# Kernel optimization log

Hardware: AMD Instinct MI355X
Metric: run time of the kernel (lower is better)

The kernel has to match this reference:

```python
import jax, jax.numpy as jnp
import numpy as np

N_NODES = 40000
N_EDGES = 640000
F_IN = 128
HID = 128
N_CLASSES = 10
N_GRAPHS = 64


def _gcn_conv(x, row, col, norm, W, b, n_nodes):
    h = x @ W                                   # [N, H]
    msg = h[row] * norm[:, None]                # [E+N, H] gather + scale
    out = jax.ops.segment_sum(msg, col, num_segments=n_nodes)  # scatter-add
    return out + b


def setup_inputs() -> dict:
    key = jax.random.key(0)
    ks = jax.random.split(key, 8)
    x = jax.random.normal(ks[0], (N_NODES, F_IN), dtype=jnp.float32)
    edge_index = jax.random.randint(ks[1], (2, N_EDGES), 0, N_NODES, dtype=jnp.int32)
    batch = jnp.sort(jax.random.randint(ks[2], (N_NODES,), 0, N_GRAPHS, dtype=jnp.int32))
    s1 = 1.0 / np.sqrt(F_IN)
    s2 = 1.0 / np.sqrt(HID)
    W1 = jax.random.normal(ks[3], (F_IN, HID), dtype=jnp.float32) * s1
    W2 = jax.random.normal(ks[4], (HID, HID), dtype=jnp.float32) * s2
    W3 = jax.random.normal(ks[5], (HID, HID), dtype=jnp.float32) * s2
    Wl = jax.random.normal(ks[6], (HID, N_CLASSES), dtype=jnp.float32) * s2
    b1 = jnp.zeros((HID,), jnp.float32)
    b2 = jnp.zeros((HID,), jnp.float32)
    b3 = jnp.zeros((HID,), jnp.float32)
    bl = jnp.zeros((N_CLASSES,), jnp.float32)
    return {"x": x, "edge_index": edge_index, "batch": batch,
            "W1": W1, "b1": b1, "W2": W2, "b2": b2, "W3": W3, "b3": b3,
            "Wl": Wl, "bl": bl}


def reference(x, edge_index, batch, W1, b1, W2, b2, W3, b3, Wl, bl):
    n = x.shape[0]
    # add self-loops (PyG add_remaining_self_loops with weight 1)
    loops = jnp.arange(n, dtype=edge_index.dtype)
    row = jnp.concatenate([edge_index[0], loops])
    col = jnp.concatenate([edge_index[1], loops])
    w = jnp.ones(row.shape, dtype=x.dtype)
    # symmetric normalization: deg over target nodes incl. self-loops
    deg = jax.ops.segment_sum(w, col, num_segments=n)
    dis = jnp.where(deg > 0, jax.lax.rsqrt(deg), 0.0)
    norm = dis[row] * dis[col]                  # [E+N]

    h = jax.nn.relu(_gcn_conv(x, row, col, norm, W1, b1, n))
    h = jax.nn.relu(_gcn_conv(h, row, col, norm, W2, b2, n))
    h = jax.nn.relu(_gcn_conv(h, row, col, norm, W3, b3, n))

    # global mean pool over graph ids
    sums = jax.ops.segment_sum(h, batch, num_segments=N_GRAPHS)      # [G, H]
    cnts = jax.ops.segment_sum(jnp.ones((n,), h.dtype), batch, num_segments=N_GRAPHS)
    pooled = sums / jnp.maximum(cnts, 1.0)[:, None]
    # dropout(p=0.2) is identity in eval mode
    return pooled @ Wl + bl                     # [G, num_classes]
```

## Files before the change

kernel.cpp:

```cpp
#include <hip/hip_runtime.h>
#include <hip/hip_bf16.h>

#define N_NODES   40000
#define N_EDGES   640000
#define F         128
#define N_GRAPHS  64
#define N_CLASSES 10

typedef short bf16x8 __attribute__((ext_vector_type(8)));
typedef float f32x4  __attribute__((ext_vector_type(4)));

__device__ __forceinline__ unsigned short f2bf(float f) {
    union { float f; unsigned u; } v; v.f = f;
    unsigned r = v.u + 0x7fffu + ((v.u >> 16) & 1u);
    return (unsigned short)(r >> 16);
}
__device__ __forceinline__ float bflo(unsigned u) { return __uint_as_float(u << 16); }
__device__ __forceinline__ float bfhi(unsigned u) { return __uint_as_float(u & 0xffff0000u); }
__device__ __forceinline__ unsigned pack2(float a, float b) {
    return (unsigned)f2bf(a) | ((unsigned)f2bf(b) << 16);
}

#define APITCH 136

__global__ void wcvt_kernel(const float* __restrict__ W1, const float* __restrict__ W2,
                            const float* __restrict__ W3, unsigned short* __restrict__ Wt,
                            int* __restrict__ deg, int* __restrict__ tks) {
    int idx = blockIdx.x * 256 + threadIdx.x;
    if (idx < N_NODES) deg[idx] = 0;
    if (idx < 2) tks[idx] = 0;
    int l = idx >> 14;
    int r = idx & 16383;
    int c = r >> 7, k = r & 127;
    const float* W = (l == 0) ? W1 : ((l == 1) ? W2 : W3);
    Wt[idx] = f2bf(W[k * 128 + c]);
}

#define SCAN_BLOCKS 40
#define SCAN_CHUNK  1000
__global__ __launch_bounds__(256) void scan_kernel(
    const int* __restrict__ deg, int* __restrict__ rowptr,
    int* __restrict__ cursor, float* __restrict__ dis,
    float* __restrict__ pooled_zero, int* __restrict__ chunkSum,
    int* __restrict__ ticket) {
    __shared__ int wpart[4];
    __shared__ int blockBase;
    const int tid  = threadIdx.x;
    const int lane = tid & 63;
    const int wave = tid >> 6;
    const int b    = blockIdx.x;
    const int base = b * SCAN_CHUNK;

    for (int k = b * 256 + tid; k < N_GRAPHS * F + N_GRAPHS; k += SCAN_BLOCKS * 256)
        pooled_zero[k] = 0.f;

    int4 d = make_int4(0, 0, 0, 0);
    if (tid < 250) d = *(const int4*)(deg + base + tid * 4);
    const int sown = d.x + d.y + d.z + d.w;

    int s = sown;
#pragma unroll
    for (int off = 1; off < 64; off <<= 1) {
        int n = __shfl_up(s, off, 64);
        if (lane >= off) s += n;
    }
    if (lane == 63) wpart[wave] = s;
    __syncthreads();

    if (tid == 0) {
        int run = 0;
#pragma unroll
        for (int w = 0; w < 4; ++w) { int t = wpart[w]; wpart[w] = run; run += t; }
        atomicExch(&chunkSum[b], run);
        __threadfence();
        atomicAdd(ticket, 1);
        while (atomicAdd(ticket, 0) < SCAN_BLOCKS) { }
    }
    __syncthreads();

    if (wave == 0) {
        int cs = (lane < SCAN_BLOCKS) ? atomicAdd(&chunkSum[lane], 0) : 0;
        int sc_ = cs;
#pragma unroll
        for (int off = 1; off < 64; off <<= 1) {
            int n = __shfl_up(sc_, off, 64);
            if (lane >= off) sc_ += n;
        }
        int bb = __shfl(sc_, (b == 0) ? 0 : b - 1, 64);
        if (lane == 0) blockBase = (b == 0) ? 0 : bb;
    }
    __syncthreads();

    if (tid < 250) {
        int excl = blockBase + wpart[wave] + (s - sown);
        int4 r;
        r.x = excl;
        r.y = r.x + d.x;
        r.z = r.y + d.y;
        r.w = r.z + d.z;
        *(int4*)(rowptr + base + tid * 4) = r;
        *(int4*)(cursor + base + tid * 4) = r;
        float4 di;
        di.x = rsqrtf((float)d.x + 1.0f);
        di.y = rsqrtf((float)d.y + 1.0f);
        di.z = rsqrtf((float)d.z + 1.0f);
        di.w = rsqrtf((float)d.w + 1.0f);
        *(float4*)(dis + base + tid * 4) = di;
    }
}

__global__ void fill_kernel(const int* __restrict__ row, const int* __restrict__ col,
                            int* __restrict__ cursor, int* __restrict__ csr_src) {
    int e = blockIdx.x * 256 + threadIdx.x;
    if (e < N_EDGES) {
        int pos = atomicAdd(&cursor[col[e]], 1);
        csr_src[pos] = row[e];
    }
}

template<bool ABF16, bool RELU, bool SCALE, bool COUNT>
__global__ __launch_bounds__(256) void gemm_mfma(
    const void* __restrict__ Araw, const unsigned short* __restrict__ Wt,
    const float* __restrict__ bias, const float* __restrict__ dis,
    unsigned short* __restrict__ Hb,
    const int* __restrict__ cnt_col, int* __restrict__ cnt_deg) {
    __shared__ unsigned short As[64 * APITCH];
    __shared__ unsigned short Ws[64 * APITCH];
    const int tid  = threadIdx.x;
    const int row0 = blockIdx.x * 64;

    if (COUNT) {
        int t = (blockIdx.x * 256 + tid) * 4;
#pragma unroll
        for (int j = 0; j < 4; ++j) atomicAdd(&cnt_deg[cnt_col[t + j]], 1);
    }

    {
        const uint4* src = (const uint4*)Wt;
#pragma unroll
        for (int j = 0; j < 4; ++j) {
            int c4 = tid + j * 256;
            int c  = c4 >> 4;
            int o  = c4 & 15;
            *(uint4*)(Ws + c * APITCH + o * 8) = src[c4];
        }
    }
    if (ABF16) {
        const uint4* src = (const uint4*)Araw;
#pragma unroll
        for (int j = 0; j < 4; ++j) {
            int c4 = tid + j * 256;
            int r  = c4 >> 4;
            int p  = c4 & 15;
            int o  = p << 3;
            uint4 hv = src[(size_t)(row0 + r) * 16 + p];
            float f0 = bflo(hv.x), f1 = bfhi(hv.x), f2 = bflo(hv.y), f3 = bfhi(hv.y);
            float f4_ = bflo(hv.z), f5 = bfhi(hv.z), f6 = bflo(hv.w), f7 = bfhi(hv.w);
            if (bias) {
                float4 b0 = *(const float4*)(bias + o);
                float4 b1 = *(const float4*)(bias + o + 4);
                f0 += b0.x; f1 += b0.y; f2 += b0.z; f3 += b0.w;
                f4_ += b1.x; f5 += b1.y; f6 += b1.z; f7 += b1.w;
            }
            if (RELU) {
                f0 = fmaxf(f0, 0.f); f1 = fmaxf(f1, 0.f); f2 = fmaxf(f2, 0.f);
                f3 = fmaxf(f3, 0.f); f4_ = fmaxf(f4_, 0.f); f5 = fmaxf(f5, 0.f);
                f6 = fmaxf(f6, 0.f); f7 = fmaxf(f7, 0.f);
            }
            uint4 pk;
            pk.x = pack2(f0, f1); pk.y = pack2(f2, f3);
            pk.z = pack2(f4_, f5); pk.w = pack2(f6, f7);
            *(uint4*)(As + r * APITCH + o) = pk;
        }
    } else {
        const float* A = (const float*)Araw;
#pragma unroll
        for (int j = 0; j < 8; ++j) {
            int c4 = tid + j * 256;
            int r  = c4 >> 5;
            int o  = (c4 & 31) << 2;
            float4 v = *(const float4*)(A + (size_t)(row0 + r) * F + o);
            if (bias) {
                v.x += bias[o + 0]; v.y += bias[o + 1];
                v.z += bias[o + 2]; v.w += bias[o + 3];
            }
            if (RELU) {
                v.x = fmaxf(v.x, 0.f); v.y = fmaxf(v.y, 0.f);
                v.z = fmaxf(v.z, 0.f); v.w = fmaxf(v.w, 0.f);
            }
            uint2 p;
            p.x = pack2(v.x, v.y);
            p.y = pack2(v.z, v.w);
            *(uint2*)(As + r * APITCH + o) = p;
        }
    }
    __syncthreads();

    const int lane = tid & 63;
    const int wave = tid >> 6;
    const int m16  = lane & 15;
    const int quad = lane >> 4;

    f32x4 acc[8];
#pragma unroll
    for (int t = 0; t < 8; ++t) acc[t] = (f32x4)(0.0f);

    bf16x8 afrag[4];
#pragma unroll
    for (int kk = 0; kk < 4; ++kk)
        afrag[kk] = *(const bf16x8*)(As + (wave * 16 + m16) * APITCH + kk * 32 + quad * 8);

#pragma unroll
    for (int kk = 0; kk < 4; ++kk) {
#pragma unroll
        for (int t = 0; t < 4; ++t) {
            bf16x8 b = *(const bf16x8*)(Ws + (t * 16 + m16) * APITCH + kk * 32 + quad * 8);
            acc[t] = __builtin_amdgcn_mfma_f32_16x16x32_bf16(afrag[kk], b, acc[t], 0, 0, 0);
        }
    }
    __syncthreads();

    {
        const uint4* src = (const uint4*)Wt + 1024;
#pragma unroll
        for (int j = 0; j < 4; ++j) {
            int c4 = tid + j * 256;
            int c  = c4 >> 4;
            int o  = c4 & 15;
            *(uint4*)(Ws + c * APITCH + o * 8) = src[c4];
        }
    }
    __syncthreads();

#pragma unroll
    for (int kk = 0; kk < 4; ++kk) {
#pragma unroll
        for (int t = 0; t < 4; ++t) {
            bf16x8 b = *(const bf16x8*)(Ws + (t * 16 + m16) * APITCH + kk * 32 + quad * 8);
            acc[4 + t] = __builtin_amdgcn_mfma_f32_16x16x32_bf16(afrag[kk], b, acc[4 + t], 0, 0, 0);
        }
    }

    const int rloc = wave * 16 + quad * 4;
    float sc[4];
#pragma unroll
    for (int rg = 0; rg < 4; ++rg) sc[rg] = SCALE ? dis[row0 + rloc + rg] : 1.0f;
#pragma unroll
    for (int t = 0; t < 8; ++t) {
        int col = t * 16 + m16;
#pragma unroll
        for (int rg = 0; rg < 4; ++rg)
            As[(rloc + rg) * APITCH + col] = f2bf(acc[t][rg] * sc[rg]);
    }
#pragma unroll
    for (int i = 0; i < 4; ++i) {
        int idx = lane + i * 64;
        int r   = idx >> 4;
        int p   = idx & 15;
        uint4 val = *(const uint4*)(As + (wave * 16 + r) * APITCH + p * 8);
        *((uint4*)(Hb + (size_t)(row0 + wave * 16 + r) * F) + p) = val;
    }
}

template <bool SCALED>
__global__ __launch_bounds__(256) void gather_kernel(
    const unsigned short* __restrict__ Hb, const int* __restrict__ csr_src,
    const int* __restrict__ rowptr, const int* __restrict__ deg,
    const float* __restrict__ dis, unsigned short* __restrict__ AGGb) {
    const int gid  = blockIdx.x * 256 + threadIdx.x;
    const int v    = gid >> 6;
    if (v >= N_NODES) return;
    const int lane = threadIdx.x & 63;
    const int part = lane & 15;
    const int quad = lane >> 4;

    const int start = rowptr[v];
    const int len   = deg[v];
    const uint4* Hp = (const uint4*)Hb + part;

    float acc[8];
#pragma unroll
    for (int i = 0; i < 8; ++i) acc[i] = 0.f;

    for (int j0 = 0; j0 < len; j0 += 64) {
        int m = len - j0; if (m > 64) m = 64;
        int nidx = (lane < m) ? csr_src[start + j0 + lane] : 0;
        for (int j = 0; j < m; j += 16) {
            int   r[4];
            float w[4];
            uint4 h[4];
#pragma unroll
            for (int u = 0; u < 4; ++u) {
                int  sl    = j + u * 4 + quad;
                bool valid = sl < m;
                r[u] = __shfl(nidx, valid ? sl : 0, 64);
                w[u] = valid ? (SCALED ? dis[r[u]] : 1.0f) : 0.0f;
            }
#pragma unroll
            for (int u = 0; u < 4; ++u) h[u] = Hp[(size_t)r[u] * 16];
#pragma unroll
            for (int u = 0; u < 4; ++u) {
                acc[0] = fmaf(bflo(h[u].x), w[u], acc[0]);
                acc[1] = fmaf(bfhi(h[u].x), w[u], acc[1]);
                acc[2] = fmaf(bflo(h[u].y), w[u], acc[2]);
                acc[3] = fmaf(bfhi(h[u].y), w[u], acc[3]);
                acc[4] = fmaf(bflo(h[u].z), w[u], acc[4]);
                acc[5] = fmaf(bfhi(h[u].z), w[u], acc[5]);
                acc[6] = fmaf(bflo(h[u].w), w[u], acc[6]);
                acc[7] = fmaf(bfhi(h[u].w), w[u], acc[7]);
            }
        }
    }

#pragma unroll
    for (int i = 0; i < 8; ++i) {
        acc[i] += __shfl_xor(acc[i], 16, 64);
        acc[i] += __shfl_xor(acc[i], 32, 64);
    }

    if (quad == 0) {
        float dc  = dis[v];
        float ws_ = SCALED ? dc : 1.0f;
        uint4 h = Hp[(size_t)v * 16];
        acc[0] = fmaf(bflo(h.x), ws_, acc[0]); acc[1] = fmaf(bfhi(h.x), ws_, acc[1]);
        acc[2] = fmaf(bflo(h.y), ws_, acc[2]); acc[3] = fmaf(bfhi(h.y), ws_, acc[3]);
        acc[4] = fmaf(bflo(h.z), ws_, acc[4]); acc[5] = fmaf(bfhi(h.z), ws_, acc[5]);
        acc[6] = fmaf(bflo(h.w), ws_, acc[6]); acc[7] = fmaf(bfhi(h.w), ws_, acc[7]);
        uint4 pk;
        pk.x = pack2(acc[0] * dc, acc[1] * dc);
        pk.y = pack2(acc[2] * dc, acc[3] * dc);
        pk.z = pack2(acc[4] * dc, acc[5] * dc);
        pk.w = pack2(acc[6] * dc, acc[7] * dc);
        *((uint4*)AGGb + (size_t)v * 16 + part) = pk;
    }
}

#define POOL_NODES 100
__global__ __launch_bounds__(256) void pool_kernel(
    const unsigned short* __restrict__ AGGb, const int* __restrict__ batch,
    const float* __restrict__ b3,
    float* __restrict__ pooled, float* __restrict__ cnt) {
    const int tid  = threadIdx.x;
    const int f4   = (tid & 31) << 2;
    const int slot = tid >> 5;
    const int base = blockIdx.x * POOL_NODES;
    const float4 bf = *(const float4*)(b3 + f4);

    float4 acc = make_float4(0.f, 0.f, 0.f, 0.f);
    float c = 0.f;
    int gcur = -1;
    for (int j = slot; j < POOL_NODES; j += 8) {
        int v = base + j;
        int g = batch[v];
        if (g != gcur) {
            if (gcur >= 0) {
                float* dst = pooled + gcur * F + f4;
                atomicAdd(dst + 0, acc.x); atomicAdd(dst + 1, acc.y);
                atomicAdd(dst + 2, acc.z); atomicAdd(dst + 3, acc.w);
                if (f4 == 0) atomicAdd(&cnt[gcur], c);
            }
            acc = make_float4(0.f, 0.f, 0.f, 0.f); c = 0.f; gcur = g;
        }
        uint2 a = *(const uint2*)(AGGb + (size_t)v * F + f4);
        acc.x += fmaxf(bflo(a.x) + bf.x, 0.f);
        acc.y += fmaxf(bfhi(a.x) + bf.y, 0.f);
        acc.z += fmaxf(bflo(a.y) + bf.z, 0.f);
        acc.w += fmaxf(bfhi(a.y) + bf.w, 0.f);
        c += 1.f;
    }
    if (gcur >= 0) {
        float* dst = pooled + gcur * F + f4;
        atomicAdd(dst + 0, acc.x); atomicAdd(dst + 1, acc.y);
        atomicAdd(dst + 2, acc.z); atomicAdd(dst + 3, acc.w);
        if (f4 == 0) atomicAdd(&cnt[gcur], c);
    }
}

__global__ void head_kernel(const float* __restrict__ pooled,
                            const float* __restrict__ cnt,
                            const float* __restrict__ Wl,
                            const float* __restrict__ bl,
                            float* __restrict__ out) {
    int tid = threadIdx.x;
    if (tid >= N_GRAPHS * N_CLASSES) return;
    int g = tid / N_CLASSES, c = tid % N_CLASSES;
    float acc = 0.f;
    for (int ff = 0; ff < F; ++ff)
        acc += pooled[g * F + ff] * Wl[ff * N_CLASSES + c];
    out[g * N_CLASSES + c] = acc / fmaxf(cnt[g], 1.f) + bl[c];
}

extern "C" void kernel_launch(void* const* d_in, const int* in_sizes, int n_in,
                              void* d_out, int out_size, void* d_ws, size_t ws_size,
                              hipStream_t stream) {
    const float* x    = (const float*)d_in[0];
    const int*   ei   = (const int*)d_in[1];
    const int*   bat  = (const int*)d_in[2];
    const float* W1   = (const float*)d_in[3];
    const float* b1   = (const float*)d_in[4];
    const float* W2   = (const float*)d_in[5];
    const float* b2   = (const float*)d_in[6];
    const float* W3   = (const float*)d_in[7];
    const float* b3   = (const float*)d_in[8];
    const float* Wl   = (const float*)d_in[9];
    const float* bl   = (const float*)d_in[10];
    float* out = (float*)d_out;

    const int* row = ei;
    const int* col = ei + N_EDGES;

    float*          ws      = (float*)d_ws;
    float*          dis     = ws;
    unsigned short* Hb      = (unsigned short*)(dis + N_NODES);
    unsigned short* AGGb    = Hb + (size_t)N_NODES * F;
    float*          pooled  = (float*)(AGGb + (size_t)N_NODES * F);
    float*          cnt     = pooled + N_GRAPHS * F;
    int*            deg     = (int*)(cnt + N_GRAPHS);
    int*            rowptr  = deg + N_NODES;
    int*            cursor  = rowptr + N_NODES;
    int*            csr_src = cursor + N_NODES;
    unsigned short* Wtb     = (unsigned short*)(csr_src + N_EDGES);
    int*            chunkSum= (int*)(Wtb + 3 * 16384);
    int*            tks     = chunkSum + SCAN_BLOCKS;

    const int edgeGrid   = (N_EDGES + 255) / 256;
    const int gemmGrid   = N_NODES / 64;
    const int gatherGrid = (N_NODES * 64) / 256;

    wcvt_kernel<<<192, 256, 0, stream>>>(W1, W2, W3, Wtb, deg, tks);

    gemm_mfma<false, false, false, true><<<gemmGrid, 256, 0, stream>>>(
        x, Wtb, nullptr, nullptr, Hb, col, deg);
    scan_kernel<<<SCAN_BLOCKS, 256, 0, stream>>>(deg, rowptr, cursor, dis,
                                                 pooled, chunkSum, &tks[0]);
    fill_kernel<<<edgeGrid, 256, 0, stream>>>(row, col, cursor, csr_src);
    gather_kernel<true><<<gatherGrid, 256, 0, stream>>>(Hb, csr_src, rowptr, deg, dis, AGGb);

    gemm_mfma<true, true, true, false><<<gemmGrid, 256, 0, stream>>>(
        AGGb, Wtb + 16384, b1, dis, Hb, nullptr, nullptr);
    gather_kernel<false><<<gatherGrid, 256, 0, stream>>>(Hb, csr_src, rowptr, deg, dis, AGGb);

    gemm_mfma<true, true, true, false><<<gemmGrid, 256, 0, stream>>>(
        AGGb, Wtb + 32768, b2, dis, Hb, nullptr, nullptr);
    gather_kernel<false><<<gatherGrid, 256, 0, stream>>>(Hb, csr_src, rowptr, deg, dis, AGGb);

    pool_kernel<<<N_NODES / POOL_NODES, 256, 0, stream>>>(AGGb, bat, b3, pooled, cnt);
    head_kernel<<<1, N_GRAPHS * N_CLASSES, 0, stream>>>(pooled, cnt, Wl, bl, out);
}
```

Baseline: 292.6 us.

## Split feature matrices into two column panels and gather each panel separately

Hb and AGGb are stored as two 64-column panels instead of row-major 128-wide rows. The gather kernel runs two passes, one per panel, so each gathered row is 128 bytes and each wave covers 8 neighbours per step. The panel being gathered is half the size, which should fit the random neighbour reads better in cache. The change also adds nontemporal loads for CSR indices and nontemporal stores for outputs, at the cost of twice as many rowptr/deg/index reads and an extra shuffle reduction step.

```diff
diff --git a/kernel.cpp b/kernel.cpp
--- a/kernel.cpp
+++ b/kernel.cpp
@@ -9,6 +9,7 @@
 
 typedef short bf16x8 __attribute__((ext_vector_type(8)));
 typedef float f32x4  __attribute__((ext_vector_type(4)));
+typedef unsigned int u32x4 __attribute__((ext_vector_type(4)));
 
 __device__ __forceinline__ unsigned short f2bf(float f) {
     union { float f; unsigned u; } v; v.f = f;
@@ -22,6 +23,8 @@
 }
 
 #define APITCH 136
+
+#define PANEL_U4  ((size_t)N_NODES * 8)
 
 __global__ void wcvt_kernel(const float* __restrict__ W1, const float* __restrict__ W2,
                             const float* __restrict__ W3, unsigned short* __restrict__ Wt,
@@ -153,7 +156,7 @@
             int r  = c4 >> 4;
             int p  = c4 & 15;
             int o  = p << 3;
-            uint4 hv = src[(size_t)(row0 + r) * 16 + p];
+            uint4 hv = src[(size_t)(p >> 3) * PANEL_U4 + (size_t)(row0 + r) * 8 + (p & 7)];
             float f0 = bflo(hv.x), f1 = bfhi(hv.x), f2 = bflo(hv.y), f3 = bfhi(hv.y);
             float f4_ = bflo(hv.z), f5 = bfhi(hv.z), f6 = bflo(hv.w), f7 = bfhi(hv.w);
             if (bias) {
@@ -258,7 +261,8 @@
         int r   = idx >> 4;
         int p   = idx & 15;
         uint4 val = *(const uint4*)(As + (wave * 16 + r) * APITCH + p * 8);
-        *((uint4*)(Hb + (size_t)(row0 + wave * 16 + r) * F) + p) = val;
+        *((uint4*)Hb + (size_t)(p >> 3) * PANEL_U4
+                     + (size_t)(row0 + wave * 16 + r) * 8 + (p & 7)) = val;
     }
 }
 
@@ -267,16 +271,16 @@
     const unsigned short* __restrict__ Hb, const int* __restrict__ csr_src,
     const int* __restrict__ rowptr, const int* __restrict__ deg,
     const float* __restrict__ dis, unsigned short* __restrict__ AGGb) {
-    const int gid  = blockIdx.x * 256 + threadIdx.x;
-    const int v    = gid >> 6;
-    if (v >= N_NODES) return;
+    const int pass = (blockIdx.x >= 10000) ? 1 : 0;
+    const int b    = blockIdx.x - pass * 10000;
+    const int v    = b * 4 + (threadIdx.x >> 6);
     const int lane = threadIdx.x & 63;
-    const int part = lane & 15;
-    const int quad = lane >> 4;
+    const int c8   = lane & 7;
+    const int oct  = lane >> 3;
 
     const int start = rowptr[v];
     const int len   = deg[v];
-    const uint4* Hp = (const uint4*)Hb + part;
+    const uint4* Hp = (const uint4*)Hb + (size_t)pass * PANEL_U4 + c8;
 
     float acc[8];
 #pragma unroll
@@ -284,20 +288,20 @@
 
     for (int j0 = 0; j0 < len; j0 += 64) {
         int m = len - j0; if (m > 64) m = 64;
-        int nidx = (lane < m) ? csr_src[start + j0 + lane] : 0;
-        for (int j = 0; j < m; j += 16) {
+        int nidx = (lane < m) ? __builtin_nontemporal_load(csr_src + start + j0 + lane) : 0;
+        for (int j = 0; j < m; j += 32) {
             int   r[4];
             float w[4];
             uint4 h[4];
 #pragma unroll
             for (int u = 0; u < 4; ++u) {
-                int  sl    = j + u * 4 + quad;
+                int  sl    = j + u * 8 + oct;
                 bool valid = sl < m;
                 r[u] = __shfl(nidx, valid ? sl : 0, 64);
                 w[u] = valid ? (SCALED ? dis[r[u]] : 1.0f) : 0.0f;
             }
 #pragma unroll
-            for (int u = 0; u < 4; ++u) h[u] = Hp[(size_t)r[u] * 16];
+            for (int u = 0; u < 4; ++u) h[u] = Hp[(size_t)r[u] * 8];
 #pragma unroll
             for (int u = 0; u < 4; ++u) {
                 acc[0] = fmaf(bflo(h[u].x), w[u], acc[0]);
@@ -314,24 +318,26 @@
 
 #pragma unroll
     for (int i = 0; i < 8; ++i) {
+        acc[i] += __shfl_xor(acc[i], 8, 64);
         acc[i] += __shfl_xor(acc[i], 16, 64);
         acc[i] += __shfl_xor(acc[i], 32, 64);
     }
 
-    if (quad == 0) {
+    if (oct == 0) {
         float dc  = dis[v];
         float ws_ = SCALED ? dc : 1.0f;
-        uint4 h = Hp[(size_t)v * 16];
+        uint4 h = Hp[(size_t)v * 8];
         acc[0] = fmaf(bflo(h.x), ws_, acc[0]); acc[1] = fmaf(bfhi(h.x), ws_, acc[1]);
         acc[2] = fmaf(bflo(h.y), ws_, acc[2]); acc[3] = fmaf(bfhi(h.y), ws_, acc[3]);
         acc[4] = fmaf(bflo(h.z), ws_, acc[4]); acc[5] = fmaf(bfhi(h.z), ws_, acc[5]);
         acc[6] = fmaf(bflo(h.w), ws_, acc[6]); acc[7] = fmaf(bfhi(h.w), ws_, acc[7]);
-        uint4 pk;
+        u32x4 pk;
         pk.x = pack2(acc[0] * dc, acc[1] * dc);
         pk.y = pack2(acc[2] * dc, acc[3] * dc);
         pk.z = pack2(acc[4] * dc, acc[5] * dc);
         pk.w = pack2(acc[6] * dc, acc[7] * dc);
-        *((uint4*)AGGb + (size_t)v * 16 + part) = pk;
+        u32x4* dst = (u32x4*)((uint4*)AGGb + (size_t)pass * PANEL_U4 + (size_t)v * 8 + c8);
+        __builtin_nontemporal_store(pk, dst);
     }
 }
 
@@ -345,6 +351,7 @@
     const int slot = tid >> 5;
     const int base = blockIdx.x * POOL_NODES;
     const float4 bf = *(const float4*)(b3 + f4);
+    const unsigned short* Ap = AGGb + (size_t)(f4 >> 6) * N_NODES * 64 + (f4 & 63);
 
     float4 acc = make_float4(0.f, 0.f, 0.f, 0.f);
     float c = 0.f;
@@ -361,7 +368,7 @@
             }
             acc = make_float4(0.f, 0.f, 0.f, 0.f); c = 0.f; gcur = g;
         }
-        uint2 a = *(const uint2*)(AGGb + (size_t)v * F + f4);
+        uint2 a = *(const uint2*)(Ap + (size_t)v * 64);
         acc.x += fmaxf(bflo(a.x) + bf.x, 0.f);
         acc.y += fmaxf(bfhi(a.x) + bf.y, 0.f);
         acc.z += fmaxf(bflo(a.y) + bf.z, 0.f);
@@ -425,7 +432,7 @@
 
     const int edgeGrid   = (N_EDGES + 255) / 256;
     const int gemmGrid   = N_NODES / 64;
-    const int gatherGrid = (N_NODES * 64) / 256;
+    const int gatherGrid = 20000;
 
     wcvt_kernel<<<192, 256, 0, stream>>>(W1, W2, W3, Wtb, deg, tks);
 
```

Result: slower. 331.6 us (+13.3%).
